# Kernel tuning notes

Measured on AMD Instinct MI355X. Metric: run time of the kernel, lower is better.

Reference implementation:

```python
import jax, jax.numpy as jnp
import numpy as np

G = 4
N = G * G  # 16 nodes

def _edges():
    e = []
    for i in range(G):
        for j in range(G):
            n = i * G + j
            if j + 1 < G:
                e += [[n, n + 1], [n + 1, n]]
            if i + 1 < G:
                e += [[n, n + G], [n + G, n]]
    # PyG GATConv default add_self_loops=True
    e += [[k, k] for k in range(N)]
    a = np.asarray(e, dtype=np.int32)
    return jnp.asarray(a[:, 0]), jnp.asarray(a[:, 1])

SRC, DST = _edges()  # [E]=64 each


def gat_layer(h, W, att_src, att_dst, bias, concat):
    # h: [B, N, Fin]; W: [Fin, H*C]; att_*: [H, C]
    B = h.shape[0]
    H, C = att_src.shape
    x = (h @ W).reshape(B, N, H, C)
    a_s = (x * att_src).sum(-1)  # [B, N, H]
    a_d = (x * att_dst).sum(-1)
    alpha = jax.nn.leaky_relu(a_s[:, SRC] + a_d[:, DST], negative_slope=0.2)  # [B, E, H]
    alpha = jnp.swapaxes(alpha, 0, 1)  # [E, B, H] (segment ops act on axis 0)
    m = jax.ops.segment_max(alpha, DST, num_segments=N)  # [N, B, H]
    ex = jnp.exp(alpha - m[DST])
    s = jax.ops.segment_sum(ex, DST, num_segments=N)
    w = ex / s[DST]  # softmax over incoming edges per dst node
    msg = w[..., None] * jnp.swapaxes(x, 0, 1)[SRC]  # [E, B, H, C]
    agg = jax.ops.segment_sum(msg, DST, num_segments=N)  # [N, B, H, C]
    agg = jnp.swapaxes(agg, 0, 1)  # [B, N, H, C]
    if concat:
        return agg.reshape(B, N, H * C) + bias
    return agg.mean(axis=2) + bias


def layer_norm(x, g, b, eps=1e-5):
    mu = x.mean(-1, keepdims=True)
    var = ((x - mu) ** 2).mean(-1, keepdims=True)
    return (x - mu) * jax.lax.rsqrt(var + eps) * g + b


def setup_inputs() -> dict:
    key = jax.random.key(0)
    ks = iter(jax.random.split(key, 32))
    B, Cin, Hd, Hh, Dout = 8192, 16, 64, 4, 256
    def gl(k, shape, fan_in):
        return jax.random.normal(k, shape, jnp.float32) * (1.0 / np.sqrt(fan_in))
    inp = {
        'x': jax.random.normal(next(ks), (B, Cin, G, G), jnp.float32),
        'w_in': gl(next(ks), (Cin, Hd), Cin),
        'b_in': jnp.zeros((Hd,), jnp.float32),
        # GAT layer 0: 64 -> 4x64 concat
        'w0': gl(next(ks), (Hd, Hh * Hd), Hd),
        'as0': gl(next(ks), (Hh, Hd), Hd), 'ad0': gl(next(ks), (Hh, Hd), Hd),
        'bias0': jnp.zeros((Hh * Hd,), jnp.float32),
        # GAT layer 1: 256 -> 4x64 concat
        'w1': gl(next(ks), (Hh * Hd, Hh * Hd), Hh * Hd),
        'as1': gl(next(ks), (Hh, Hd), Hd), 'ad1': gl(next(ks), (Hh, Hd), Hd),
        'bias1': jnp.zeros((Hh * Hd,), jnp.float32),
        # GAT layer 2: 256 -> 64 (mean over heads)
        'w2': gl(next(ks), (Hh * Hd, Hh * Hd), Hh * Hd),
        'as2': gl(next(ks), (Hh, Hd), Hd), 'ad2': gl(next(ks), (Hh, Hd), Hd),
        'bias2': jnp.zeros((Hd,), jnp.float32),
        # output MLP: 64 -> 128 -> 256, LN+ReLU after each layer
        'mw1': gl(next(ks), (Hd, Dout // 2), Hd), 'mb1': jnp.zeros((Dout // 2,), jnp.float32),
        'g1': jnp.ones((Dout // 2,), jnp.float32), 'be1': jnp.zeros((Dout // 2,), jnp.float32),
        'mw2': gl(next(ks), (Dout // 2, Dout), Dout // 2), 'mb2': jnp.zeros((Dout,), jnp.float32),
        'g2': jnp.ones((Dout,), jnp.float32), 'be2': jnp.zeros((Dout,), jnp.float32),
    }
    return inp


def reference(x, w_in, b_in, w0, as0, ad0, bias0, w1, as1, ad1, bias1,
              w2, as2, ad2, bias2, mw1, mb1, g1, be1, mw2, mb2, g2, be2):
    B = x.shape[0]
    # grid -> node features: (B,C,H,W) -> (B,H,W,C) -> (B,N,C)
    h = jnp.transpose(x, (0, 2, 3, 1)).reshape(B, N, -1)
    h = jax.nn.relu(h @ w_in + b_in)
    h = gat_layer(h, w0, as0, ad0, bias0, concat=True)
    h = jax.nn.relu(h)  # dropout inactive in eval
    h = gat_layer(h, w1, as1, ad1, bias1, concat=True)
    h = jax.nn.relu(h)
    h = gat_layer(h, w2, as2, ad2, bias2, concat=False)  # [B, N, 64]
    gr = h.mean(axis=1)  # global mean pool over the 16 nodes
    y = jax.nn.relu(layer_norm(gr @ mw1 + mb1, g1, be1))
    y = jax.nn.relu(layer_norm(y @ mw2 + mb2, g2, be2))
    return y
```

## Files before the change

### kernel.cpp

```cpp
#include <hip/hip_runtime.h>
#include <hip/hip_bf16.h>

typedef unsigned short u16;
typedef unsigned int   u32;
typedef __attribute__((ext_vector_type(8)))  short bf16x8;
typedef __attribute__((ext_vector_type(16))) float f32x16;

#define GPB 4
#define ZERO16 (f32x16){0.f,0.f,0.f,0.f,0.f,0.f,0.f,0.f,0.f,0.f,0.f,0.f,0.f,0.f,0.f,0.f}
#define MFMA32 __builtin_amdgcn_mfma_f32_32x32x16_bf16

__constant__ int ADJ_DEG[16] = {3,4,4,3, 4,5,5,4, 4,5,5,4, 3,4,4,3};
__constant__ int ADJ_SRC[16][5] = {
  {0,1,4,0,0},   {1,0,2,5,0},   {2,1,3,6,0},   {3,2,7,0,0},
  {4,5,0,8,0},   {5,4,6,1,9},   {6,5,7,2,10},  {7,6,3,11,0},
  {8,9,4,12,0},  {9,8,10,5,13}, {10,9,11,6,14},{11,10,7,15,0},
  {12,13,8,0,0}, {13,12,14,9,0},{14,13,15,10,0},{15,14,11,0,0}
};

struct SMem {
  char hA[64*512];
  char hBT[4*256*32];
  union {
    struct { float asd[64][8]; char ptb[16*16*32]; } post;
    struct { float grs[4][64]; float z1[4][128]; float red[2][8][2]; } mlp;
  } u;
};

__device__ __forceinline__ int swz(int row, int b) {
  return (row << 9) + (b ^ ((row & 7) << 4) ^ (((row >> 3) & 1) << 5));
}
__device__ __forceinline__ int xswz(int g, int c, int b) {
  return (g << 13) + (c << 5) + (b ^ (((c >> 2) & 1) << 4) ^ (((c >> 3) & 1) << 3));
}
__device__ __forceinline__ int ptbx(int g, int h, int d, int b) {
  return (((g*4 + h)*16 + d) << 5) + (b ^ (((h ^ (d >> 2)) & 1) << 4));
}
__device__ __forceinline__ u32 f2bf1(float x) {
  u32 u = __float_as_uint(x);
  return (u + 0x7fffu + ((u >> 16) & 1u)) >> 16;
}
__device__ __forceinline__ u32 pk2(float a, float b) {
  __hip_bfloat162 h2 = __float22bfloat162_rn(make_float2(a, b));
  union { __hip_bfloat162 h; u32 u; } cv; cv.h = h2; return cv.u;
}
__device__ __forceinline__ bf16x8 hbt_read(const SMem& sm, int g, int c, int hi) {
  union { uint2 u2[2]; bf16x8 v; } cv;
  cv.u2[0] = *(const uint2*)(sm.hBT + xswz(g, c, hi*16));
  cv.u2[1] = *(const uint2*)(sm.hBT + xswz(g, c, hi*16 + 8));
  return cv.v;
}

template<int KS>
__device__ __forceinline__ void gemm32(SMem& sm, const uint4* __restrict__ wsrc, int t) {
  const int lane = t & 63, w = t >> 6;
  const int l31 = lane & 31, hi = lane >> 5;
  const bool hasAtt = (w < 2);

  f32x16 acc0 = ZERO16, acc1 = ZERO16, accA = ZERO16;

#pragma unroll 4
  for (int ks = 0; ks < KS; ++ks) {
    const uint4 bw = wsrc[(ks*9 + w)*64 + lane];
    uint4 ba;
    if (hasAtt) ba = wsrc[(ks*9 + 8)*64 + lane];
    const bf16x8 a0 = *(const bf16x8*)(sm.hA + swz(l31,      ks*32 + hi*16));
    const bf16x8 a1 = *(const bf16x8*)(sm.hA + swz(32 + l31, ks*32 + hi*16));
    acc0 = MFMA32(a0, *(const bf16x8*)&bw, acc0, 0, 0, 0);
    acc1 = MFMA32(a1, *(const bf16x8*)&bw, acc1, 0, 0, 0);
    if (hasAtt) accA = MFMA32((w == 0) ? a0 : a1, *(const bf16x8*)&ba, accA, 0, 0, 0);
  }

  const int c = w*32 + l31;
#pragma unroll
  for (int mh = 0; mh < 2; ++mh) {
    const f32x16 A = mh ? acc1 : acc0;
#pragma unroll
    for (int grp = 0; grp < 4; ++grp) {
      const int g  = mh*2 + (grp >> 1);
      const int n0 = (grp & 1)*8 + hi*4;
      uint2 o;
      o.x = pk2(A[grp*4+0], A[grp*4+1]);
      o.y = pk2(A[grp*4+2], A[grp*4+3]);
      *(uint2*)(sm.hBT + xswz(g, c, n0*2)) = o;
    }
  }

  if (hasAtt) {
    if (l31 < 8) {
#pragma unroll
      for (int grp = 0; grp < 4; ++grp) {
        const int g  = w*2 + (grp >> 1);
        const int n0 = (grp & 1)*8 + hi*4;
#pragma unroll
        for (int i = 0; i < 4; ++i)
          sm.u.post.asd[g*16 + n0 + i][l31] = accA[grp*4+i];
      }
    }
    const int g = w*2 + hi;
    const int h = lane & 3;
#pragma unroll
    for (int dd = 0; dd < 2; ++dd) {
      const int d = ((lane >> 2) & 7) + dd*8;
      const int deg = ADJ_DEG[d];
      const float advl = sm.u.post.asd[g*16 + d][4 + h];
      float al[5]; int srcs[5];
      float m = -1e30f;
#pragma unroll
      for (int k = 0; k < 5; ++k) {
        srcs[k] = (k < deg) ? ADJ_SRC[d][k] : 99;
        float v = 0.f;
        if (k < deg) {
          v = sm.u.post.asd[g*16 + srcs[k]][h] + advl;
          v = (v > 0.f) ? v : 0.2f * v;
          m = fmaxf(m, v);
        }
        al[k] = v;
      }
      float ssum = 0.f;
#pragma unroll
      for (int k = 0; k < 5; ++k)
        if (k < deg) { const float e = __expf(al[k] - m); al[k] = e; ssum += e; }
      const float inv = 1.f / ssum;
      float p[16];
#pragma unroll
      for (int s = 0; s < 16; ++s) {
        float v = 0.f;
#pragma unroll
        for (int k = 0; k < 5; ++k) v = (srcs[k] == s) ? al[k] * inv : v;
        p[s] = v;
      }
      uint4 lo, hh;
      lo.x = pk2(p[0],p[1]);   lo.y = pk2(p[2],p[3]);   lo.z = pk2(p[4],p[5]);   lo.w = pk2(p[6],p[7]);
      hh.x = pk2(p[8],p[9]);   hh.y = pk2(p[10],p[11]); hh.z = pk2(p[12],p[13]); hh.w = pk2(p[14],p[15]);
      *(uint4*)(sm.u.post.ptb + ptbx(g, h, d, 0))  = lo;
      *(uint4*)(sm.u.post.ptb + ptbx(g, h, d, 16)) = hh;
    }
  }
}

template<int MODE>
__device__ __forceinline__ void agg32(SMem& sm, const float* __restrict__ bias, int t) {
  const int lane = t & 63, w = t >> 6;
  const int l31 = lane & 31, hi = lane >> 5;
  const int g = w >> 1;
  const bf16x8 zero8 = {0,0,0,0,0,0,0,0};

  if (MODE == 0) {
#pragma unroll
    for (int i = 0; i < 4; ++i) {
      const int mt = (w & 1)*4 + i;
      const int h = mt >> 1;
      bf16x8 pb = zero8;
      if (l31 < 16)
        pb = *(const bf16x8*)(sm.u.post.ptb + ptbx(g, h, l31, hi*16));
      const bf16x8 a = hbt_read(sm, g, mt*32 + l31, hi);
      f32x16 acc = ZERO16;
      acc = MFMA32(a, pb, acc, 0, 0, 0);
      if (l31 < 16) {
        const int row = g*16 + l31;
#pragma unroll
        for (int grp = 0; grp < 4; ++grp) {
          const int cb = mt*32 + grp*8 + hi*4;
          const float4 bv = *(const float4*)(bias + cb);
          uint2 o;
          o.x = pk2(fmaxf(acc[grp*4+0] + bv.x, 0.f), fmaxf(acc[grp*4+1] + bv.y, 0.f));
          o.y = pk2(fmaxf(acc[grp*4+2] + bv.z, 0.f), fmaxf(acc[grp*4+3] + bv.w, 0.f));
          *(uint2*)(sm.hA + swz(row, 2*cb)) = o;
        }
      }
    }
  } else {
    const int mt = w & 1;
    f32x16 acc = ZERO16;
#pragma unroll
    for (int h = 0; h < 4; ++h) {
      bf16x8 pb = zero8;
      if (l31 < 16)
        pb = *(const bf16x8*)(sm.u.post.ptb + ptbx(g, h, l31, hi*16));
      const bf16x8 a = hbt_read(sm, g, h*64 + mt*32 + l31, hi);
      acc = MFMA32(a, pb, acc, 0, 0, 0);
    }
#pragma unroll
    for (int i = 0; i < 16; ++i) {
      acc[i] += __shfl_xor(acc[i], 1);
      acc[i] += __shfl_xor(acc[i], 2);
      acc[i] += __shfl_xor(acc[i], 4);
      acc[i] += __shfl_xor(acc[i], 8);
    }
    if (l31 < 4) {
      float4 ov;
      if (l31 == 0)      { ov.x = acc[0];  ov.y = acc[1];  ov.z = acc[2];  ov.w = acc[3];  }
      else if (l31 == 1) { ov.x = acc[4];  ov.y = acc[5];  ov.z = acc[6];  ov.w = acc[7];  }
      else if (l31 == 2) { ov.x = acc[8];  ov.y = acc[9];  ov.z = acc[10]; ov.w = acc[11]; }
      else               { ov.x = acc[12]; ov.y = acc[13]; ov.z = acc[14]; ov.w = acc[15]; }
      const int c0 = mt*32 + l31*8 + hi*4;
      const float4 bv = *(const float4*)(bias + c0);
      ov.x = fmaf(1.f/64.f, ov.x, bv.x);
      ov.y = fmaf(1.f/64.f, ov.y, bv.y);
      ov.z = fmaf(1.f/64.f, ov.z, bv.z);
      ov.w = fmaf(1.f/64.f, ov.w, bv.w);
      *(float4*)&sm.u.mlp.grs[g][c0] = ov;
    }
  }
}

extern "C" __global__ void __launch_bounds__(512, 4)
gat_main(const float* __restrict__ xg, const float* __restrict__ b_in,
         const float* __restrict__ bias0, const float* __restrict__ bias1,
         const float* __restrict__ bias2,
         const uint4* __restrict__ wq0, const uint4* __restrict__ wq1,
         const uint4* __restrict__ wq2, const uint4* __restrict__ winq,
         const float* __restrict__ mw1, const float* __restrict__ mb1,
         const float* __restrict__ g1, const float* __restrict__ be1,
         const u32* __restrict__ mwb2, const float* __restrict__ mb2,
         const float* __restrict__ g2, const float* __restrict__ be2,
         float* __restrict__ out, int Btot)
{
  __shared__ SMem sm;
  const int t = threadIdx.x;
  const int b0 = blockIdx.x * GPB;
  if (b0 >= Btot) return;
  const int lane = t & 63, w = t >> 6;
  const int l31 = lane & 31, hi = lane >> 5;

  if (w < 4) {
    const int mtC = w & 1, ntN = w >> 1;
    const int gg = ntN*2 + (l31 >> 4), node = l31 & 15;
    float xv[8];
#pragma unroll
    for (int j = 0; j < 8; ++j)
      xv[j] = xg[(size_t)(b0 + gg)*256 + (hi*8 + j)*16 + node];
    union { u32 uu[4]; bf16x8 v; } bcv;
#pragma unroll
    for (int j = 0; j < 4; ++j) bcv.uu[j] = pk2(xv[2*j], xv[2*j+1]);
    const uint4 aw4 = winq[mtC*64 + lane];
    f32x16 acc = ZERO16;
    acc = MFMA32(*(const bf16x8*)&aw4, bcv.v, acc, 0, 0, 0);
    const int row = ntN*32 + l31;
#pragma unroll
    for (int grp = 0; grp < 4; ++grp) {
      const int cb = mtC*32 + grp*8 + hi*4;
      const float4 bv = *(const float4*)(b_in + cb);
      uint2 o;
      o.x = pk2(fmaxf(acc[grp*4+0] + bv.x, 0.f), fmaxf(acc[grp*4+1] + bv.y, 0.f));
      o.y = pk2(fmaxf(acc[grp*4+2] + bv.z, 0.f), fmaxf(acc[grp*4+3] + bv.w, 0.f));
      *(uint2*)(sm.hA + swz(row, 2*cb)) = o;
    }
  }
  __syncthreads();

  gemm32<4>(sm, wq0, t);   __syncthreads();
  agg32<0>(sm, bias0, t);  __syncthreads();

  gemm32<16>(sm, wq1, t);  __syncthreads();
  agg32<0>(sm, bias1, t);  __syncthreads();

  gemm32<16>(sm, wq2, t);  __syncthreads();
  agg32<1>(sm, bias2, t);  __syncthreads();

  const int mg = t >> 7, o = t & 127;
  float a1v = mb1[o];
#pragma unroll 8
  for (int k = 0; k < 64; ++k) a1v = fmaf(sm.u.mlp.grs[mg][k], mw1[k*128 + o], a1v);
  {
    float su = a1v, sq = a1v*a1v;
#pragma unroll
    for (int off = 32; off >= 1; off >>= 1) { su += __shfl_xor(su, off); sq += __shfl_xor(sq, off); }
    if (lane == 0) { sm.u.mlp.red[0][w][0] = su; sm.u.mlp.red[0][w][1] = sq; }
  }
  __syncthreads();
  {
    const float mu = (sm.u.mlp.red[0][2*mg][0] + sm.u.mlp.red[0][2*mg+1][0]) * (1.f/128.f);
    const float mq = (sm.u.mlp.red[0][2*mg][1] + sm.u.mlp.red[0][2*mg+1][1]) * (1.f/128.f);
    const float rstd = rsqrtf(mq - mu*mu + 1e-5f);
    sm.u.mlp.z1[mg][o] = fmaxf((a1v - mu)*rstd*g1[o] + be1[o], 0.f);
  }
  __syncthreads();

  {
    const float2 bb2 = *(const float2*)(mb2 + 2*o);
    float c0 = bb2.x, c1 = bb2.y;
#pragma unroll 8
    for (int k = 0; k < 128; ++k) {
      const float zk = sm.u.mlp.z1[mg][k];
      const u32 uw = mwb2[k*128 + o];
      c0 = fmaf(zk, __uint_as_float(uw << 16), c0);
      c1 = fmaf(zk, __uint_as_float(uw & 0xffff0000u), c1);
    }
    float su = c0 + c1, sq = c0*c0 + c1*c1;
#pragma unroll
    for (int off = 32; off >= 1; off >>= 1) { su += __shfl_xor(su, off); sq += __shfl_xor(sq, off); }
    if (lane == 0) { sm.u.mlp.red[1][w][0] = su; sm.u.mlp.red[1][w][1] = sq; }
    __syncthreads();
    const float mu = (sm.u.mlp.red[1][2*mg][0] + sm.u.mlp.red[1][2*mg+1][0]) * (1.f/256.f);
    const float mq = (sm.u.mlp.red[1][2*mg][1] + sm.u.mlp.red[1][2*mg+1][1]) * (1.f/256.f);
    const float rstd = rsqrtf(mq - mu*mu + 1e-5f);
    const float2 gg2  = *(const float2*)(g2  + 2*o);
    const float2 bbe2 = *(const float2*)(be2 + 2*o);
    float2 ov;
    ov.x = fmaxf((c0 - mu)*rstd*gg2.x + bbe2.x, 0.f);
    ov.y = fmaxf((c1 - mu)*rstd*gg2.y + bbe2.y, 0.f);
    *(float2*)(out + (size_t)(b0 + mg)*256 + 2*o) = ov;
  }
}

__global__ void __launch_bounds__(256)
prep_w(const float* __restrict__ w0, const float* __restrict__ as0, const float* __restrict__ ad0,
       const float* __restrict__ w1, const float* __restrict__ as1, const float* __restrict__ ad1,
       const float* __restrict__ w2, const float* __restrict__ as2, const float* __restrict__ ad2,
       const float* __restrict__ w_in, const float* __restrict__ mw2, u16* __restrict__ wf) {
  const int f = blockIdx.x*256 + threadIdx.x;
  if (f >= 199680) return;
  if (f >= 166912) { wf[f] = (u16)f2bf1(mw2[f - 166912]); return; }
  if (f >= 165888) {
    const int local = f - 165888;
    const int nt = local >> 9, lane = (local >> 3) & 63, j = local & 7;
    wf[f] = (u16)f2bf1(w_in[((lane >> 5)*8 + j)*64 + nt*32 + (lane & 31)]);
    return;
  }
  const float *W, *as_, *ad_; int local;
  if (f < 18432)      { W = w0; as_ = as0; ad_ = ad0; local = f; }
  else if (f < 92160) { W = w1; as_ = as1; ad_ = ad1; local = f - 18432; }
  else                { W = w2; as_ = as2; ad_ = ad2; local = f - 92160; }
  const int ks = local / 4608;
  const int r  = local - ks*4608;
  const int nt = r >> 9;
  const int lane = (r >> 3) & 63;
  const int j = r & 7;
  const int k = ks*16 + (lane >> 5)*8 + j;
  const int col = lane & 31;
  float val;
  if (nt < 8) {
    val = W[k*256 + nt*32 + col];
  } else if (col < 8) {
    const int h = col & 3;
    const float* av = (col < 4) ? as_ : ad_;
    float s = 0.f;
    for (int c = 0; c < 64; ++c) s = fmaf(W[k*256 + h*64 + c], av[h*64 + c], s);
    val = s;
  } else {
    val = 0.f;
  }
  wf[f] = (u16)f2bf1(val);
}

extern "C" void kernel_launch(void* const* d_in, const int* in_sizes, int n_in,
                              void* d_out, int out_size, void* d_ws, size_t ws_size,
                              hipStream_t stream) {
  (void)n_in; (void)out_size; (void)ws_size;
  const float* xg   = (const float*)d_in[0];
  const float* w_in = (const float*)d_in[1];
  const float* b_in = (const float*)d_in[2];
  const float* w0   = (const float*)d_in[3];
  const float* as0  = (const float*)d_in[4];
  const float* ad0  = (const float*)d_in[5];
  const float* bi0  = (const float*)d_in[6];
  const float* w1   = (const float*)d_in[7];
  const float* as1  = (const float*)d_in[8];
  const float* ad1  = (const float*)d_in[9];
  const float* bi1  = (const float*)d_in[10];
  const float* w2   = (const float*)d_in[11];
  const float* as2  = (const float*)d_in[12];
  const float* ad2  = (const float*)d_in[13];
  const float* bi2  = (const float*)d_in[14];
  const float* mw1  = (const float*)d_in[15];
  const float* mb1  = (const float*)d_in[16];
  const float* g1   = (const float*)d_in[17];
  const float* be1  = (const float*)d_in[18];
  const float* mw2  = (const float*)d_in[19];
  const float* mb2  = (const float*)d_in[20];
  const float* g2   = (const float*)d_in[21];
  const float* be2  = (const float*)d_in[22];
  float* out = (float*)d_out;

  const int Btot = in_sizes[0] / 256;
  u16* wf = (u16*)d_ws;
  const uint4* wq0  = (const uint4*)wf;
  const uint4* wq1  = (const uint4*)(wf + 18432);
  const uint4* wq2  = (const uint4*)(wf + 92160);
  const uint4* winq = (const uint4*)(wf + 165888);
  const u32*   mwb2 = (const u32*)(wf + 166912);

  hipLaunchKernelGGL(prep_w, dim3(780), dim3(256), 0, stream,
                     w0, as0, ad0, w1, as1, ad1, w2, as2, ad2, w_in, mw2, wf);

  const int nblocks = (Btot + GPB - 1) / GPB;
  hipLaunchKernelGGL(gat_main, dim3(nblocks), dim3(512), 0, stream,
                     xg, b_in, bi0, bi1, bi2, wq0, wq1, wq2, winq,
                     mw1, mb1, g1, be1, mwb2, mb2, g2, be2, out, Btot);
}
```

Baseline: 152.9 us.

## Split MLP head out of GAT kernel into a separate launch

Moves the pooled-graph MLP with its two layer norms out of the fused GAT kernel into its own kernel. The GAT kernel now writes the pooled features to a workspace buffer in global memory. This shortens the main kernel, cuts its register and shared-memory pressure, and removes its tail barriers, which may raise occupancy. In exchange it adds an extra kernel launch and a round trip of the pooled features through global memory.

```diff
diff --git a/kernel.cpp b/kernel.cpp
--- a/kernel.cpp
+++ b/kernel.cpp
@@ -21,10 +21,7 @@
 struct SMem {
   char hA[64*512];
   char hBT[4*256*32];
-  union {
-    struct { float asd[64][8]; char ptb[16*16*32]; } post;
-    struct { float grs[4][64]; float z1[4][128]; float red[2][8][2]; } mlp;
-  } u;
+  struct { float asd[64][8]; char ptb[16*16*32]; } post;
 };
 
 __device__ __forceinline__ int swz(int row, int b) {
@@ -94,7 +91,7 @@
         const int n0 = (grp & 1)*8 + hi*4;
 #pragma unroll
         for (int i = 0; i < 4; ++i)
-          sm.u.post.asd[g*16 + n0 + i][l31] = accA[grp*4+i];
+          sm.post.asd[g*16 + n0 + i][l31] = accA[grp*4+i];
       }
     }
     const int g = w*2 + hi;
@@ -103,7 +100,7 @@
     for (int dd = 0; dd < 2; ++dd) {
       const int d = ((lane >> 2) & 7) + dd*8;
       const int deg = ADJ_DEG[d];
-      const float advl = sm.u.post.asd[g*16 + d][4 + h];
+      const float advl = sm.post.asd[g*16 + d][4 + h];
       float al[5]; int srcs[5];
       float m = -1e30f;
 #pragma unroll
@@ -111,7 +108,7 @@
         srcs[k] = (k < deg) ? ADJ_SRC[d][k] : 99;
         float v = 0.f;
         if (k < deg) {
-          v = sm.u.post.asd[g*16 + srcs[k]][h] + advl;
+          v = sm.post.asd[g*16 + srcs[k]][h] + advl;
           v = (v > 0.f) ? v : 0.2f * v;
           m = fmaxf(m, v);
         }
@@ -133,14 +130,15 @@
       uint4 lo, hh;
       lo.x = pk2(p[0],p[1]);   lo.y = pk2(p[2],p[3]);   lo.z = pk2(p[4],p[5]);   lo.w = pk2(p[6],p[7]);
       hh.x = pk2(p[8],p[9]);   hh.y = pk2(p[10],p[11]); hh.z = pk2(p[12],p[13]); hh.w = pk2(p[14],p[15]);
-      *(uint4*)(sm.u.post.ptb + ptbx(g, h, d, 0))  = lo;
-      *(uint4*)(sm.u.post.ptb + ptbx(g, h, d, 16)) = hh;
+      *(uint4*)(sm.post.ptb + ptbx(g, h, d, 0))  = lo;
+      *(uint4*)(sm.post.ptb + ptbx(g, h, d, 16)) = hh;
     }
   }
 }
 
 template<int MODE>
-__device__ __forceinline__ void agg32(SMem& sm, const float* __restrict__ bias, int t) {
+__device__ __forceinline__ void agg32(SMem& sm, const float* __restrict__ bias, int t,
+                                      float* __restrict__ gr, int b0) {
   const int lane = t & 63, w = t >> 6;
   const int l31 = lane & 31, hi = lane >> 5;
   const int g = w >> 1;
@@ -153,7 +151,7 @@
       const int h = mt >> 1;
       bf16x8 pb = zero8;
       if (l31 < 16)
-        pb = *(const bf16x8*)(sm.u.post.ptb + ptbx(g, h, l31, hi*16));
+        pb = *(const bf16x8*)(sm.post.ptb + ptbx(g, h, l31, hi*16));
       const bf16x8 a = hbt_read(sm, g, mt*32 + l31, hi);
       f32x16 acc = ZERO16;
       acc = MFMA32(a, pb, acc, 0, 0, 0);
@@ -177,7 +175,7 @@
     for (int h = 0; h < 4; ++h) {
       bf16x8 pb = zero8;
       if (l31 < 16)
-        pb = *(const bf16x8*)(sm.u.post.ptb + ptbx(g, h, l31, hi*16));
+        pb = *(const bf16x8*)(sm.post.ptb + ptbx(g, h, l31, hi*16));
       const bf16x8 a = hbt_read(sm, g, h*64 + mt*32 + l31, hi);
       acc = MFMA32(a, pb, acc, 0, 0, 0);
     }
@@ -200,7 +198,7 @@
       ov.y = fmaf(1.f/64.f, ov.y, bv.y);
       ov.z = fmaf(1.f/64.f, ov.z, bv.z);
       ov.w = fmaf(1.f/64.f, ov.w, bv.w);
-      *(float4*)&sm.u.mlp.grs[g][c0] = ov;
+      *(float4*)(gr + (size_t)(b0 + g)*64 + c0) = ov;
     }
   }
 }
@@ -211,11 +209,7 @@
          const float* __restrict__ bias2,
          const uint4* __restrict__ wq0, const uint4* __restrict__ wq1,
          const uint4* __restrict__ wq2, const uint4* __restrict__ winq,
-         const float* __restrict__ mw1, const float* __restrict__ mb1,
-         const float* __restrict__ g1, const float* __restrict__ be1,
-         const u32* __restrict__ mwb2, const float* __restrict__ mb2,
-         const float* __restrict__ g2, const float* __restrict__ be2,
-         float* __restrict__ out, int Btot)
+         float* __restrict__ gr, int Btot)
 {
   __shared__ SMem sm;
   const int t = threadIdx.x;
@@ -250,31 +244,49 @@
   }
   __syncthreads();
 
-  gemm32<4>(sm, wq0, t);   __syncthreads();
-  agg32<0>(sm, bias0, t);  __syncthreads();
-
-  gemm32<16>(sm, wq1, t);  __syncthreads();
-  agg32<0>(sm, bias1, t);  __syncthreads();
-
-  gemm32<16>(sm, wq2, t);  __syncthreads();
-  agg32<1>(sm, bias2, t);  __syncthreads();
-
-  const int mg = t >> 7, o = t & 127;
+  gemm32<4>(sm, wq0, t);            __syncthreads();
+  agg32<0>(sm, bias0, t, gr, b0);   __syncthreads();
+
+  gemm32<16>(sm, wq1, t);           __syncthreads();
+  agg32<0>(sm, bias1, t, gr, b0);   __syncthreads();
+
+  gemm32<16>(sm, wq2, t);           __syncthreads();
+  agg32<1>(sm, bias2, t, gr, b0);
+}
+
+extern "C" __global__ void __launch_bounds__(512)
+mlp_kernel(const float* __restrict__ mw1, const float* __restrict__ mb1,
+           const float* __restrict__ g1, const float* __restrict__ be1,
+           const u32* __restrict__ mwb2, const float* __restrict__ mb2,
+           const float* __restrict__ g2, const float* __restrict__ be2,
+           const float* __restrict__ gr, float* __restrict__ out, int Btot)
+{
+  __shared__ float grs[4][64];
+  __shared__ float z1[4][128];
+  __shared__ float red[2][8][2];
+  const int t = threadIdx.x;
+  const int b0 = blockIdx.x * 4;
+  if (b0 >= Btot) return;
+  if (t < 256) grs[t >> 6][t & 63] = gr[(size_t)b0*64 + t];
+  __syncthreads();
+
+  const int mg = t >> 7, o = t & 127, w = t >> 6, lane = t & 63;
+
   float a1v = mb1[o];
 #pragma unroll 8
-  for (int k = 0; k < 64; ++k) a1v = fmaf(sm.u.mlp.grs[mg][k], mw1[k*128 + o], a1v);
+  for (int k = 0; k < 64; ++k) a1v = fmaf(grs[mg][k], mw1[k*128 + o], a1v);
   {
     float su = a1v, sq = a1v*a1v;
 #pragma unroll
     for (int off = 32; off >= 1; off >>= 1) { su += __shfl_xor(su, off); sq += __shfl_xor(sq, off); }
-    if (lane == 0) { sm.u.mlp.red[0][w][0] = su; sm.u.mlp.red[0][w][1] = sq; }
+    if (lane == 0) { red[0][w][0] = su; red[0][w][1] = sq; }
   }
   __syncthreads();
   {
-    const float mu = (sm.u.mlp.red[0][2*mg][0] + sm.u.mlp.red[0][2*mg+1][0]) * (1.f/128.f);
-    const float mq = (sm.u.mlp.red[0][2*mg][1] + sm.u.mlp.red[0][2*mg+1][1]) * (1.f/128.f);
+    const float mu = (red[0][2*mg][0] + red[0][2*mg+1][0]) * (1.f/128.f);
+    const float mq = (red[0][2*mg][1] + red[0][2*mg+1][1]) * (1.f/128.f);
     const float rstd = rsqrtf(mq - mu*mu + 1e-5f);
-    sm.u.mlp.z1[mg][o] = fmaxf((a1v - mu)*rstd*g1[o] + be1[o], 0.f);
+    z1[mg][o] = fmaxf((a1v - mu)*rstd*g1[o] + be1[o], 0.f);
   }
   __syncthreads();
 
@@ -283,7 +295,7 @@
     float c0 = bb2.x, c1 = bb2.y;
 #pragma unroll 8
     for (int k = 0; k < 128; ++k) {
-      const float zk = sm.u.mlp.z1[mg][k];
+      const float zk = z1[mg][k];
       const u32 uw = mwb2[k*128 + o];
       c0 = fmaf(zk, __uint_as_float(uw << 16), c0);
       c1 = fmaf(zk, __uint_as_float(uw & 0xffff0000u), c1);
@@ -291,10 +303,10 @@
     float su = c0 + c1, sq = c0*c0 + c1*c1;
 #pragma unroll
     for (int off = 32; off >= 1; off >>= 1) { su += __shfl_xor(su, off); sq += __shfl_xor(sq, off); }
-    if (lane == 0) { sm.u.mlp.red[1][w][0] = su; sm.u.mlp.red[1][w][1] = sq; }
+    if (lane == 0) { red[1][w][0] = su; red[1][w][1] = sq; }
     __syncthreads();
-    const float mu = (sm.u.mlp.red[1][2*mg][0] + sm.u.mlp.red[1][2*mg+1][0]) * (1.f/256.f);
-    const float mq = (sm.u.mlp.red[1][2*mg][1] + sm.u.mlp.red[1][2*mg+1][1]) * (1.f/256.f);
+    const float mu = (red[1][2*mg][0] + red[1][2*mg+1][0]) * (1.f/256.f);
+    const float mq = (red[1][2*mg][1] + red[1][2*mg+1][1]) * (1.f/256.f);
     const float rstd = rsqrtf(mq - mu*mu + 1e-5f);
     const float2 gg2  = *(const float2*)(g2  + 2*o);
     const float2 bbe2 = *(const float2*)(be2 + 2*o);
@@ -381,12 +393,15 @@
   const uint4* wq2  = (const uint4*)(wf + 92160);
   const uint4* winq = (const uint4*)(wf + 165888);
   const u32*   mwb2 = (const u32*)(wf + 166912);
+  float* gr = (float*)((char*)d_ws + 401408);
 
   hipLaunchKernelGGL(prep_w, dim3(780), dim3(256), 0, stream,
                      w0, as0, ad0, w1, as1, ad1, w2, as2, ad2, w_in, mw2, wf);
 
   const int nblocks = (Btot + GPB - 1) / GPB;
   hipLaunchKernelGGL(gat_main, dim3(nblocks), dim3(512), 0, stream,
-                     xg, b_in, bi0, bi1, bi2, wq0, wq1, wq2, winq,
-                     mw1, mb1, g1, be1, mwb2, mb2, g2, be2, out, Btot);
-}
+                     xg, b_in, bi0, bi1, bi2, wq0, wq1, wq2, winq, gr, Btot);
+
+  hipLaunchKernelGGL(mlp_kernel, dim3((Btot + 3) / 4), dim3(512), 0, stream,
+                     mw1, mb1, g1, be1, mwb2, mb2, g2, be2, gr, out, Btot);
+}
```

After: 151.5 us. No clear change (-0.9%).
